# Optimization experiments

Measured on AMD Instinct MI355X. Metric: run time of the kernel, lower is better.

The kernel has to match this reference:

```python
import jax, jax.numpy as jnp
import numpy as np

CHANNELS = 512
NUM_HEADS = 8
NUM_GROUPS = 32
EPS = 1e-5


def setup_inputs() -> dict:
    key = jax.random.key(0)
    ks = jax.random.split(key, 6)
    c = CHANNELS
    x = jax.random.normal(ks[0], (8, c, 32, 32), dtype=jnp.float32)
    norm_w = jnp.ones((c,), jnp.float32)
    norm_b = jnp.zeros((c,), jnp.float32)
    # 1x1 conv1d weights stored as [out, in]
    qkv_w = jax.random.normal(ks[1], (3 * c, c), jnp.float32) * (1.0 / np.sqrt(c))
    qkv_b = jax.random.normal(ks[2], (3 * c,), jnp.float32) * 0.02
    # proj_out is zero-initialized in the original; use small random values so the
    # residual branch is exercised numerically (init values are not part of the math).
    proj_w = jax.random.normal(ks[3], (c, c), jnp.float32) * 0.02
    proj_b = jax.random.normal(ks[4], (c,), jnp.float32) * 0.02
    return {"x": x, "norm_w": norm_w, "norm_b": norm_b,
            "qkv_w": qkv_w, "qkv_b": qkv_b, "proj_w": proj_w, "proj_b": proj_b}


def _group_norm(x, w, b):
    # x: [B, C, L]; normalize per (batch, group) over (C/G, L) in float32
    B, C, L = x.shape
    xg = x.astype(jnp.float32).reshape(B, NUM_GROUPS, (C // NUM_GROUPS) * L)
    mean = xg.mean(axis=-1, keepdims=True)
    var = xg.var(axis=-1, keepdims=True)
    xn = ((xg - mean) * jax.lax.rsqrt(var + EPS)).reshape(B, C, L)
    return (xn * w[None, :, None] + b[None, :, None]).astype(x.dtype)


def _attention_legacy(qkv, n_heads):
    # qkv: [B, 3*C, L]  (QKVAttentionLegacy: split heads after reshape)
    B, width, L = qkv.shape
    ch = width // (3 * n_heads)
    q, k, v = jnp.split(qkv.reshape(B * n_heads, 3 * ch, L), 3, axis=1)
    scale = 1.0 / np.sqrt(np.sqrt(ch))
    w = jnp.einsum('bct,bcs->bts', q * scale, k * scale)  # [B*H, L, L]
    w = jax.nn.softmax(w.astype(jnp.float32), axis=-1).astype(qkv.dtype)
    a = jnp.einsum('bts,bcs->bct', w, v)  # [B*H, ch, L]
    return a.reshape(B, n_heads * ch, L)


def reference(x, norm_w, norm_b, qkv_w, qkv_b, proj_w, proj_b):
    b, c = x.shape[0], x.shape[1]
    spatial = x.shape[2:]
    x_ = x.reshape(b, c, -1)  # [B, C, L]
    xn = _group_norm(x_, norm_w, norm_b)
    qkv = jnp.einsum('oc,bcl->bol', qkv_w, xn) + qkv_b[None, :, None]
    h = _attention_legacy(qkv, NUM_HEADS)
    h = jnp.einsum('oc,bcl->bol', proj_w, h) + proj_b[None, :, None]
    return (x_ + h).reshape(b, c, *spatial)
```

## Files before the change

### kernel.cpp

```cpp
#include <hip/hip_runtime.h>
#include <hip/hip_bf16.h>
#include <stdint.h>


#define NB 8
#define NC 512
#define NL 1024
#define NHD 8
#define ND 64

typedef __attribute__((ext_vector_type(4))) float f32x4;
typedef __attribute__((ext_vector_type(8))) short bf16x8;
typedef __attribute__((ext_vector_type(4))) short bf16x4;
typedef __attribute__((ext_vector_type(4))) unsigned short u16x4;
typedef __attribute__((ext_vector_type(8))) unsigned short u16x8;

#define MFMA16(a, b, c) __builtin_amdgcn_mfma_f32_16x16x32_bf16((a), (b), (c), 0, 0, 0)

static __device__ __forceinline__ f32x4 mfma_k16(bf16x4 a, bf16x4 b, f32x4 c) {
#if __has_builtin(__builtin_amdgcn_mfma_f32_16x16x16bf16_1k)
  return __builtin_amdgcn_mfma_f32_16x16x16bf16_1k(a, b, c, 0, 0, 0);
#else
  asm("v_mfma_f32_16x16x16_bf16 %0, %1, %2, %0" : "+v"(c) : "v"(a), "v"(b));
  return c;
#endif
}

#if __has_builtin(__builtin_amdgcn_exp2f)
#define EXP2F __builtin_amdgcn_exp2f
#else
#define EXP2F exp2f
#endif

static __device__ __forceinline__ unsigned short f2bf(float f) {
  union { float f; uint32_t u; } v; v.f = f;
  uint32_t r = v.u + 0x7fffu + ((v.u >> 16) & 1u);
  return (unsigned short)(r >> 16);
}

static __device__ __forceinline__ short f2bf_h(float f) {
  __hip_bfloat16 h = __float2bfloat16(f);
  return *reinterpret_cast<short*>(&h);
}

static __device__ __forceinline__ void gl_lds16(const unsigned short* g, unsigned short* l) {
  __builtin_amdgcn_global_load_lds(
      (const __attribute__((address_space(1))) void*)g,
      (__attribute__((address_space(3))) void*)l, 16, 0, 0);
}

__global__ __launch_bounds__(256) void k_pre(const float* __restrict__ x,
                                             const float* __restrict__ nw,
                                             const float* __restrict__ nb,
                                             const float* __restrict__ qkvw,
                                             const float* __restrict__ pw,
                                             unsigned short* __restrict__ xnt,
                                             unsigned short* __restrict__ qwb,
                                             unsigned short* __restrict__ pwb) {
  if (blockIdx.x >= 256) {
    int i = (blockIdx.x - 256) * 256 + threadIdx.x;
    const int NQ4 = (3 * NC * NC) / 4;
    if (i < NQ4) {
      f32x4 v = ((const f32x4*)qkvw)[i];
      u16x4 o; o.x = f2bf(v.x); o.y = f2bf(v.y); o.z = f2bf(v.z); o.w = f2bf(v.w);
      ((u16x4*)qwb)[i] = o;
    } else {
      int j = i - NQ4;
      f32x4 v = ((const f32x4*)pw)[j];
      u16x4 o; o.x = f2bf(v.x); o.y = f2bf(v.y); o.z = f2bf(v.z); o.w = f2bf(v.w);
      ((u16x4*)pwb)[j] = o;
    }
    return;
  }
  const int b = blockIdx.x >> 5, g = blockIdx.x & 31;
  const float* base = x + ((size_t)b * NC + g * 16) * NL;
  const int t = threadIdx.x;
  f32x4 vals[16];
  float s = 0.f, ss = 0.f;
#pragma unroll
  for (int r = 0; r < 16; ++r) {
    f32x4 v = ((const f32x4*)base)[t + 256 * r];
    vals[r] = v;
    s += v.x + v.y + v.z + v.w;
    ss += v.x * v.x + v.y * v.y + v.z * v.z + v.w * v.w;
  }
#pragma unroll
  for (int m = 1; m < 64; m <<= 1) { s += __shfl_xor(s, m, 64); ss += __shfl_xor(ss, m, 64); }
  __shared__ float red[8];
  const int w = t >> 6;
  if ((t & 63) == 0) { red[w] = s; red[4 + w] = ss; }
  __syncthreads();
  s  = red[0] + red[1] + red[2] + red[3];
  ss = red[4] + red[5] + red[6] + red[7];
  const float mean = s * (1.f / 16384.f);
  const float var  = ss * (1.f / 16384.f) - mean * mean;
  const float inv  = rsqrtf(var + 1e-5f);
  u16x8 ov[4][2];
#pragma unroll
  for (int r = 0; r < 16; ++r) {
    float wcv = nw[g * 16 + r] * inv;
    float bcv = nb[g * 16 + r] - mean * wcv;
    f32x4 v = vals[r];
    ov[0][r >> 3][r & 7] = f2bf(v.x * wcv + bcv);
    ov[1][r >> 3][r & 7] = f2bf(v.y * wcv + bcv);
    ov[2][r >> 3][r & 7] = f2bf(v.z * wcv + bcv);
    ov[3][r >> 3][r & 7] = f2bf(v.w * wcv + bcv);
  }
#pragma unroll
  for (int j = 0; j < 4; ++j) {
    size_t off = ((size_t)b * NL + 4 * t + j) * NC + g * 16;
    *(u16x8*)(xnt + off)     = ov[j][0];
    *(u16x8*)(xnt + off + 8) = ov[j][1];
  }
}

__global__ __launch_bounds__(256) void k_qkv(const unsigned short* __restrict__ xnt,
                                             const unsigned short* __restrict__ qwb,
                                             const float* __restrict__ qkvb,
                                             unsigned short* __restrict__ qt,
                                             unsigned short* __restrict__ kt,
                                             unsigned short* __restrict__ vt) {
  __shared__ __align__(16) unsigned short As[128 * 64];
  __shared__ __align__(16) unsigned short Bs[128 * 64];
  const int m0 = blockIdx.x * 128;
  const int n0 = blockIdx.y * 128;
  const int b = blockIdx.z;
  const int tid = threadIdx.x, lane = tid & 63, w = tid >> 6;
  const int wr = w >> 1, wc = w & 1;

  int soff[4];
#pragma unroll
  for (int r = 0; r < 4; ++r) {
    int c = (r * 4 + w) * 64 + lane;
    int row = c >> 3, lc = (c & 7) ^ (row & 7);
    soff[r] = row * NC + lc * 8;
  }
  const unsigned short* Ap = xnt + (size_t)b * NL * NC + (size_t)m0 * NC;
  const unsigned short* Bp = qwb + (size_t)n0 * NC;

  f32x4 acc[4][4];
#pragma unroll
  for (int mi = 0; mi < 4; ++mi)
#pragma unroll
    for (int ni = 0; ni < 4; ++ni) acc[mi][ni] = (f32x4){0.f, 0.f, 0.f, 0.f};

  for (int k0 = 0; k0 < NC; k0 += 64) {
#pragma unroll
    for (int r = 0; r < 4; ++r) gl_lds16(Ap + soff[r], &As[(r * 4 + w) * 512]);
#pragma unroll
    for (int r = 0; r < 4; ++r) gl_lds16(Bp + soff[r], &Bs[(r * 4 + w) * 512]);
    Ap += 64; Bp += 64;
    __syncthreads();
#pragma unroll
    for (int ks = 0; ks < 2; ++ks) {
      bf16x8 af[4], bfr[4];
#pragma unroll
      for (int mi = 0; mi < 4; ++mi) {
        int row = wr * 64 + mi * 16 + (lane & 15);
        int ph = ((lane >> 4) + ks * 4) ^ (row & 7);
        af[mi] = *(const bf16x8*)&As[row * 64 + ph * 8];
      }
#pragma unroll
      for (int ni = 0; ni < 4; ++ni) {
        int row = wc * 64 + ni * 16 + (lane & 15);
        int ph = ((lane >> 4) + ks * 4) ^ (row & 7);
        bfr[ni] = *(const bf16x8*)&Bs[row * 64 + ph * 8];
      }
#pragma unroll
      for (int mi = 0; mi < 4; ++mi)
#pragma unroll
        for (int ni = 0; ni < 4; ++ni)
          acc[mi][ni] = MFMA16(af[mi], bfr[ni], acc[mi][ni]);
    }
    __syncthreads();
  }
#pragma unroll
  for (int ni = 0; ni < 4; ++ni) {
    int o = n0 + wc * 64 + ni * 16 + (lane & 15);
    int head = o / 192, rem = o - head * 192;
    int type = rem >> 6, ch = rem & 63;
    float bias = qkvb[o];
#pragma unroll
    for (int mi = 0; mi < 4; ++mi) {
      int l0 = m0 + wr * 64 + mi * 16 + ((lane >> 4) << 2);
      if (type == 2) {
        u16x4 pk;
#pragma unroll
        for (int i = 0; i < 4; ++i) pk[i] = f2bf(acc[mi][ni][i] + bias);
        *(u16x4*)&vt[(((size_t)(b * NHD + head) * 256 + (l0 >> 2)) * ND + ch) * 4] = pk;
      } else {
        const float sc = (type == 0)
            ? (0.35355339059327373f * 1.4426950408889634f)
            : 0.35355339059327373f;
        unsigned short* dst =
            (type == 0 ? qt : kt) + ((size_t)(b * NHD + head) * NL + l0) * ND + ch;
#pragma unroll
        for (int i = 0; i < 4; ++i)
          dst[i * ND] = f2bf((acc[mi][ni][i] + bias) * sc);
      }
    }
  }
}

__global__ __launch_bounds__(256) void k_attn(const unsigned short* __restrict__ qt,
                                              const unsigned short* __restrict__ kt,
                                              const unsigned short* __restrict__ vt,
                                              unsigned short* __restrict__ abuf) {
  __shared__ __align__(16) unsigned short Ks[2][128 * 64];
  __shared__ __align__(16) unsigned short Vs[2][128 * 64];
  const int bid = blockIdx.x;
  const int bh = (bid & 7) * 8 + (bid >> 6);
  const int tb = (bid >> 3) & 7;
  const int tid = threadIdx.x, lane = tid & 63, w = tid >> 6;
  const int lo = lane & 15, g = lane >> 4;
  const int t0 = tb * 128 + w * 32;
  const unsigned short* qb = qt + (size_t)bh * NL * ND;

  int koff[4], voff[4];
#pragma unroll
  for (int r = 0; r < 4; ++r) {
    int c = (r * 4 + w) * 64 + lane;
    int row = c >> 3, lc = (c & 7) ^ (row & 7);
    koff[r] = row * ND + lc * 8;
    voff[r] = c * 8;
  }
  const int e0 = lo * 64 + ((g ^ (lo & 7)) * 8);
  const int e1 = lo * 64 + (((4 + g) ^ (lo & 7)) * 8);
  const int vbase = g * 256 + lo * 4;

  const unsigned short* kst = kt + (size_t)bh * NL * ND;
  const unsigned short* vst = vt + (size_t)bh * NL * ND;

  bf16x8 qf[2][2];
#pragma unroll
  for (int h = 0; h < 2; ++h)
#pragma unroll
    for (int ks = 0; ks < 2; ++ks)
      qf[h][ks] = *(const bf16x8*)&qb[(size_t)(t0 + h * 16 + lo) * ND + ks * 32 + g * 8];

  bf16x4 vones;
#pragma unroll
  for (int j = 0; j < 4; ++j) vones[j] = (short)0x3F80;

  f32x4 pv[2][4];
#pragma unroll
  for (int h = 0; h < 2; ++h)
#pragma unroll
    for (int ci = 0; ci < 4; ++ci) pv[h][ci] = (f32x4){0.f, 0.f, 0.f, 0.f};
  f32x4 lacc[2];
  lacc[0] = (f32x4){0.f, 0.f, 0.f, 0.f};
  lacc[1] = (f32x4){0.f, 0.f, 0.f, 0.f};

#pragma unroll
  for (int r = 0; r < 4; ++r) {
    gl_lds16(kst + koff[r], &Ks[0][(r * 4 + w) * 512]);
    gl_lds16(vst + voff[r], &Vs[0][(r * 4 + w) * 512]);
  }
  kst += 8192; vst += 8192;

#define ATTN_HALF(BUF, HH)                                                    \
  {                                                                           \
    f32x4 sacc[2][4];                                                         \
    _Pragma("unroll")                                                         \
    for (int h = 0; h < 2; ++h)                                               \
      _Pragma("unroll")                                                       \
      for (int sblk = 0; sblk < 4; ++sblk)                                    \
        sacc[h][sblk] = (f32x4){0.f, 0.f, 0.f, 0.f};                          \
    __builtin_amdgcn_s_setprio(1);                                            \
    _Pragma("unroll")                                                         \
    for (int sblk = 0; sblk < 4; ++sblk) {                                    \
      bf16x8 kf = *(const bf16x8*)&Ks[BUF][(HH) * 4096 + sblk * 1024 + e0];   \
      sacc[0][sblk] = MFMA16(kf, qf[0][0], sacc[0][sblk]);                    \
      sacc[1][sblk] = MFMA16(kf, qf[1][0], sacc[1][sblk]);                    \
    }                                                                         \
    _Pragma("unroll")                                                         \
    for (int sblk = 0; sblk < 4; ++sblk) {                                    \
      bf16x8 kf = *(const bf16x8*)&Ks[BUF][(HH) * 4096 + sblk * 1024 + e1];   \
      sacc[0][sblk] = MFMA16(kf, qf[0][1], sacc[0][sblk]);                    \
      sacc[1][sblk] = MFMA16(kf, qf[1][1], sacc[1][sblk]);                    \
    }                                                                         \
    __builtin_amdgcn_s_setprio(0);                                            \
    _Pragma("unroll")                                                         \
    for (int sblk = 0; sblk < 4; ++sblk) {                                    \
      float a0 = EXP2F(sacc[0][sblk][0]);                                     \
      float a1 = EXP2F(sacc[0][sblk][1]);                                     \
      float a2 = EXP2F(sacc[0][sblk][2]);                                     \
      float a3 = EXP2F(sacc[0][sblk][3]);                                     \
      bf16x4 pf0;                                                             \
      pf0[0] = f2bf_h(a0); pf0[1] = f2bf_h(a1);                               \
      pf0[2] = f2bf_h(a2); pf0[3] = f2bf_h(a3);                               \
      float b0 = EXP2F(sacc[1][sblk][0]);                                     \
      float b1 = EXP2F(sacc[1][sblk][1]);                                     \
      float b2 = EXP2F(sacc[1][sblk][2]);                                     \
      float b3 = EXP2F(sacc[1][sblk][3]);                                     \
      bf16x4 pf1;                                                             \
      pf1[0] = f2bf_h(b0); pf1[1] = f2bf_h(b1);                               \
      pf1[2] = f2bf_h(b2); pf1[3] = f2bf_h(b3);                               \
      __builtin_amdgcn_s_setprio(1);                                          \
      lacc[0] = mfma_k16(pf0, vones, lacc[0]);                                \
      lacc[1] = mfma_k16(pf1, vones, lacc[1]);                                \
      _Pragma("unroll")                                                       \
      for (int ci = 0; ci < 4; ++ci) {                                        \
        bf16x4 vf = *(const bf16x4*)                                          \
            &Vs[BUF][(HH) * 4096 + sblk * 1024 + ci * 64 + vbase];            \
        pv[0][ci] = mfma_k16(pf0, vf, pv[0][ci]);                             \
        pv[1][ci] = mfma_k16(pf1, vf, pv[1][ci]);                             \
      }                                                                       \
      __builtin_amdgcn_s_setprio(0);                                          \
    }                                                                         \
  }

#define ATTN_TILE(BUF, LAST)                                                  \
  {                                                                           \
    __syncthreads();                                                          \
    if (!(LAST)) {                                                            \
      _Pragma("unroll")                                                       \
      for (int r = 0; r < 4; ++r)                                             \
        gl_lds16(kst + koff[r], &Ks[(BUF) ^ 1][(r * 4 + w) * 512]);           \
    }                                                                         \
    ATTN_HALF(BUF, 0);                                                        \
    if (!(LAST)) {                                                            \
      _Pragma("unroll")                                                       \
      for (int r = 0; r < 4; ++r)                                             \
        gl_lds16(vst + voff[r], &Vs[(BUF) ^ 1][(r * 4 + w) * 512]);           \
      kst += 8192; vst += 8192;                                               \
    }                                                                         \
    ATTN_HALF(BUF, 1);                                                        \
  }

  for (int it = 0; it < 8; it += 2) {
    ATTN_TILE(0, false);
    ATTN_TILE(1, it == 6);
  }
#undef ATTN_TILE
#undef ATTN_HALF

#pragma unroll
  for (int h = 0; h < 2; ++h) {
    float li[4];
#pragma unroll
    for (int i = 0; i < 4; ++i) li[i] = 1.0f / lacc[h][i];
#pragma unroll
    for (int ci = 0; ci < 4; ++ci)
#pragma unroll
      for (int i = 0; i < 4; ++i) {
        int tl = t0 + h * 16 + g * 4 + i;
        abuf[((size_t)bh * NL + tl) * ND + ci * 16 + lo] = f2bf_h(pv[h][ci][i] * li[i]);
      }
  }
}

__global__ __launch_bounds__(256) void k_proj(const unsigned short* __restrict__ abuf,
                                              const unsigned short* __restrict__ pwb,
                                              const float* __restrict__ pb,
                                              const float* __restrict__ x,
                                              float* __restrict__ out) {
  __shared__ __align__(16) unsigned short As[128 * 64];
  __shared__ __align__(16) unsigned short Bs[128 * 64];
  const int m0 = blockIdx.x * 128;
  const int n0 = blockIdx.y * 128;
  const int b = blockIdx.z;
  const int tid = threadIdx.x, lane = tid & 63, w = tid >> 6;
  const int wr = w >> 1, wc = w & 1;

  int aoff[4], boff[4];
#pragma unroll
  for (int r = 0; r < 4; ++r) {
    int c = (r * 4 + w) * 64 + lane;
    int row = c >> 3, lc = (c & 7) ^ (row & 7);
    aoff[r] = row * NC + lc * 8;
    boff[r] = row * ND + lc * 8;
  }
  const unsigned short* Ap = pwb + (size_t)m0 * NC;
  const unsigned short* Bp = abuf + ((size_t)(b * NHD) * NL + n0) * ND;

  f32x4 acc[4][4];
#pragma unroll
  for (int mi = 0; mi < 4; ++mi)
#pragma unroll
    for (int ni = 0; ni < 4; ++ni) acc[mi][ni] = (f32x4){0.f, 0.f, 0.f, 0.f};

  for (int k0 = 0; k0 < NC; k0 += 64) {
#pragma unroll
    for (int r = 0; r < 4; ++r) gl_lds16(Ap + aoff[r], &As[(r * 4 + w) * 512]);
#pragma unroll
    for (int r = 0; r < 4; ++r) gl_lds16(Bp + boff[r], &Bs[(r * 4 + w) * 512]);
    Ap += 64; Bp += (size_t)NL * ND;
    __syncthreads();
#pragma unroll
    for (int ks = 0; ks < 2; ++ks) {
      bf16x8 af[4], bfr[4];
#pragma unroll
      for (int mi = 0; mi < 4; ++mi) {
        int row = wr * 64 + mi * 16 + (lane & 15);
        int ph = ((lane >> 4) + ks * 4) ^ (row & 7);
        af[mi] = *(const bf16x8*)&As[row * 64 + ph * 8];
      }
#pragma unroll
      for (int ni = 0; ni < 4; ++ni) {
        int row = wc * 64 + ni * 16 + (lane & 15);
        int ph = ((lane >> 4) + ks * 4) ^ (row & 7);
        bfr[ni] = *(const bf16x8*)&Bs[row * 64 + ph * 8];
      }
#pragma unroll
      for (int mi = 0; mi < 4; ++mi)
#pragma unroll
        for (int ni = 0; ni < 4; ++ni)
          acc[mi][ni] = MFMA16(af[mi], bfr[ni], acc[mi][ni]);
    }
    __syncthreads();
  }
#pragma unroll
  for (int mi = 0; mi < 4; ++mi)
#pragma unroll
    for (int i = 0; i < 4; ++i) {
      int o = m0 + wr * 64 + mi * 16 + ((lane >> 4) << 2) + i;
      float pbv = pb[o];
#pragma unroll
      for (int ni = 0; ni < 4; ++ni) {
        int l = n0 + wc * 64 + ni * 16 + (lane & 15);
        size_t idx = ((size_t)b * NC + o) * NL + l;
        out[idx] = x[idx] + acc[mi][ni][i] + pbv;
      }
    }
}

extern "C" void kernel_launch(void* const* d_in, const int* in_sizes, int n_in,
                              void* d_out, int out_size, void* d_ws, size_t ws_size,
                              hipStream_t stream) {
  const float* x    = (const float*)d_in[0];
  const float* nw   = (const float*)d_in[1];
  const float* nb   = (const float*)d_in[2];
  const float* qkvw = (const float*)d_in[3];
  const float* qkvb = (const float*)d_in[4];
  const float* pw   = (const float*)d_in[5];
  const float* pb   = (const float*)d_in[6];
  float* out = (float*)d_out;

  char* ws = (char*)d_ws;
  unsigned short* xnt  = (unsigned short*)(ws);
  unsigned short* abuf = (unsigned short*)(ws);
  unsigned short* qwb  = (unsigned short*)(ws + 8388608);
  unsigned short* pwb  = (unsigned short*)(ws + 9961472);
  unsigned short* qt   = (unsigned short*)(ws + 10485760);
  unsigned short* kt   = (unsigned short*)(ws + 18874368);
  unsigned short* vt   = (unsigned short*)(ws + 27262976);

  k_pre<<<1280, 256, 0, stream>>>(x, nw, nb, qkvw, pw, xnt, qwb, pwb);
  k_qkv<<<dim3(8, 12, 8), 256, 0, stream>>>(xnt, qwb, qkvb, qt, kt, vt);
  k_attn<<<512, 256, 0, stream>>>(qt, kt, vt, abuf);
  k_proj<<<dim3(4, 8, 8), 256, 0, stream>>>(abuf, pwb, pb, x, out);
}
```

Before: 79.53 us.

## Double-buffer LDS tiles in QKV and projection GEMMs to overlap loads

Both the QKV and output-projection GEMM kernels now keep two LDS buffers per operand. Global-to-LDS loads for the next K-slice are issued between the MFMA sub-steps on the current buffer, and only one barrier is used per K step. The goal is to hide global load latency behind MFMA work. The cost is twice the LDS per block (64 KB), which may reduce occupancy.

```diff
diff --git a/kernel.cpp b/kernel.cpp
--- a/kernel.cpp
+++ b/kernel.cpp
@@ -120,13 +120,14 @@
                                              unsigned short* __restrict__ qt,
                                              unsigned short* __restrict__ kt,
                                              unsigned short* __restrict__ vt) {
-  __shared__ __align__(16) unsigned short As[128 * 64];
-  __shared__ __align__(16) unsigned short Bs[128 * 64];
+  __shared__ __align__(16) unsigned short As[2][128 * 64];
+  __shared__ __align__(16) unsigned short Bs[2][128 * 64];
   const int m0 = blockIdx.x * 128;
   const int n0 = blockIdx.y * 128;
   const int b = blockIdx.z;
   const int tid = threadIdx.x, lane = tid & 63, w = tid >> 6;
   const int wr = w >> 1, wc = w & 1;
+  const int lo = lane & 15, g = lane >> 4;
 
   int soff[4];
 #pragma unroll
@@ -144,45 +145,69 @@
 #pragma unroll
     for (int ni = 0; ni < 4; ++ni) acc[mi][ni] = (f32x4){0.f, 0.f, 0.f, 0.f};
 
-  for (int k0 = 0; k0 < NC; k0 += 64) {
-#pragma unroll
-    for (int r = 0; r < 4; ++r) gl_lds16(Ap + soff[r], &As[(r * 4 + w) * 512]);
-#pragma unroll
-    for (int r = 0; r < 4; ++r) gl_lds16(Bp + soff[r], &Bs[(r * 4 + w) * 512]);
-    Ap += 64; Bp += 64;
-    __syncthreads();
-#pragma unroll
-    for (int ks = 0; ks < 2; ++ks) {
-      bf16x8 af[4], bfr[4];
-#pragma unroll
-      for (int mi = 0; mi < 4; ++mi) {
-        int row = wr * 64 + mi * 16 + (lane & 15);
-        int ph = ((lane >> 4) + ks * 4) ^ (row & 7);
-        af[mi] = *(const bf16x8*)&As[row * 64 + ph * 8];
-      }
-#pragma unroll
-      for (int ni = 0; ni < 4; ++ni) {
-        int row = wc * 64 + ni * 16 + (lane & 15);
-        int ph = ((lane >> 4) + ks * 4) ^ (row & 7);
-        bfr[ni] = *(const bf16x8*)&Bs[row * 64 + ph * 8];
-      }
-#pragma unroll
-      for (int mi = 0; mi < 4; ++mi)
-#pragma unroll
-        for (int ni = 0; ni < 4; ++ni)
-          acc[mi][ni] = MFMA16(af[mi], bfr[ni], acc[mi][ni]);
-    }
-    __syncthreads();
-  }
+#pragma unroll
+  for (int r = 0; r < 4; ++r) {
+    gl_lds16(Ap + soff[r], &As[0][(r * 4 + w) * 512]);
+    gl_lds16(Bp + soff[r], &Bs[0][(r * 4 + w) * 512]);
+  }
+  Ap += 64; Bp += 64;
+
+#define QKV_KS(BUF, KS)                                                       \
+  {                                                                           \
+    bf16x8 af[4], bfr[4];                                                     \
+    _Pragma("unroll")                                                         \
+    for (int mi = 0; mi < 4; ++mi) {                                          \
+      int row = wr * 64 + mi * 16 + lo;                                       \
+      int ph = (g + (KS) * 4) ^ (row & 7);                                    \
+      af[mi] = *(const bf16x8*)&As[BUF][row * 64 + ph * 8];                   \
+    }                                                                         \
+    _Pragma("unroll")                                                         \
+    for (int ni = 0; ni < 4; ++ni) {                                          \
+      int row = wc * 64 + ni * 16 + lo;                                       \
+      int ph = (g + (KS) * 4) ^ (row & 7);                                    \
+      bfr[ni] = *(const bf16x8*)&Bs[BUF][row * 64 + ph * 8];                  \
+    }                                                                         \
+    _Pragma("unroll")                                                         \
+    for (int mi = 0; mi < 4; ++mi)                                            \
+      _Pragma("unroll")                                                       \
+      for (int ni = 0; ni < 4; ++ni)                                          \
+        acc[mi][ni] = MFMA16(af[mi], bfr[ni], acc[mi][ni]);                   \
+  }
+
+#define QKV_STEP(BUF, LAST)                                                   \
+  {                                                                           \
+    __syncthreads();                                                          \
+    if (!(LAST)) {                                                            \
+      _Pragma("unroll")                                                       \
+      for (int r = 0; r < 4; ++r)                                             \
+        gl_lds16(Ap + soff[r], &As[(BUF) ^ 1][(r * 4 + w) * 512]);            \
+    }                                                                         \
+    QKV_KS(BUF, 0);                                                           \
+    if (!(LAST)) {                                                            \
+      _Pragma("unroll")                                                       \
+      for (int r = 0; r < 4; ++r)                                             \
+        gl_lds16(Bp + soff[r], &Bs[(BUF) ^ 1][(r * 4 + w) * 512]);            \
+      Ap += 64; Bp += 64;                                                     \
+    }                                                                         \
+    QKV_KS(BUF, 1);                                                           \
+  }
+
+  for (int it = 0; it < 8; it += 2) {
+    QKV_STEP(0, false);
+    QKV_STEP(1, it == 6);
+  }
+#undef QKV_STEP
+#undef QKV_KS
+
 #pragma unroll
   for (int ni = 0; ni < 4; ++ni) {
-    int o = n0 + wc * 64 + ni * 16 + (lane & 15);
+    int o = n0 + wc * 64 + ni * 16 + lo;
     int head = o / 192, rem = o - head * 192;
     int type = rem >> 6, ch = rem & 63;
     float bias = qkvb[o];
 #pragma unroll
     for (int mi = 0; mi < 4; ++mi) {
-      int l0 = m0 + wr * 64 + mi * 16 + ((lane >> 4) << 2);
+      int l0 = m0 + wr * 64 + mi * 16 + (g << 2);
       if (type == 2) {
         u16x4 pk;
 #pragma unroll
@@ -355,13 +380,14 @@
                                               const float* __restrict__ pb,
                                               const float* __restrict__ x,
                                               float* __restrict__ out) {
-  __shared__ __align__(16) unsigned short As[128 * 64];
-  __shared__ __align__(16) unsigned short Bs[128 * 64];
+  __shared__ __align__(16) unsigned short As[2][128 * 64];
+  __shared__ __align__(16) unsigned short Bs[2][128 * 64];
   const int m0 = blockIdx.x * 128;
   const int n0 = blockIdx.y * 128;
   const int b = blockIdx.z;
   const int tid = threadIdx.x, lane = tid & 63, w = tid >> 6;
   const int wr = w >> 1, wc = w & 1;
+  const int lo = lane & 15, g = lane >> 4;
 
   int aoff[4], boff[4];
 #pragma unroll
@@ -380,45 +406,69 @@
 #pragma unroll
     for (int ni = 0; ni < 4; ++ni) acc[mi][ni] = (f32x4){0.f, 0.f, 0.f, 0.f};
 
-  for (int k0 = 0; k0 < NC; k0 += 64) {
-#pragma unroll
-    for (int r = 0; r < 4; ++r) gl_lds16(Ap + aoff[r], &As[(r * 4 + w) * 512]);
-#pragma unroll
-    for (int r = 0; r < 4; ++r) gl_lds16(Bp + boff[r], &Bs[(r * 4 + w) * 512]);
-    Ap += 64; Bp += (size_t)NL * ND;
-    __syncthreads();
-#pragma unroll
-    for (int ks = 0; ks < 2; ++ks) {
-      bf16x8 af[4], bfr[4];
-#pragma unroll
-      for (int mi = 0; mi < 4; ++mi) {
-        int row = wr * 64 + mi * 16 + (lane & 15);
-        int ph = ((lane >> 4) + ks * 4) ^ (row & 7);
-        af[mi] = *(const bf16x8*)&As[row * 64 + ph * 8];
-      }
+#pragma unroll
+  for (int r = 0; r < 4; ++r) {
+    gl_lds16(Ap + aoff[r], &As[0][(r * 4 + w) * 512]);
+    gl_lds16(Bp + boff[r], &Bs[0][(r * 4 + w) * 512]);
+  }
+  Ap += 64; Bp += (size_t)NL * ND;
+
+#define PROJ_KS(BUF, KS)                                                      \
+  {                                                                           \
+    bf16x8 af[4], bfr[4];                                                     \
+    _Pragma("unroll")                                                         \
+    for (int mi = 0; mi < 4; ++mi) {                                          \
+      int row = wr * 64 + mi * 16 + lo;                                       \
+      int ph = (g + (KS) * 4) ^ (row & 7);                                    \
+      af[mi] = *(const bf16x8*)&As[BUF][row * 64 + ph * 8];                   \
+    }                                                                         \
+    _Pragma("unroll")                                                         \
+    for (int ni = 0; ni < 4; ++ni) {                                          \
+      int row = wc * 64 + ni * 16 + lo;                                       \
+      int ph = (g + (KS) * 4) ^ (row & 7);                                    \
+      bfr[ni] = *(const bf16x8*)&Bs[BUF][row * 64 + ph * 8];                  \
+    }                                                                         \
+    _Pragma("unroll")                                                         \
+    for (int mi = 0; mi < 4; ++mi)                                            \
+      _Pragma("unroll")                                                       \
+      for (int ni = 0; ni < 4; ++ni)                                          \
+        acc[mi][ni] = MFMA16(af[mi], bfr[ni], acc[mi][ni]);                   \
+  }
+
+#define PROJ_STEP(BUF, LAST)                                                  \
+  {                                                                           \
+    __syncthreads();                                                          \
+    if (!(LAST)) {                                                            \
+      _Pragma("unroll")                                                       \
+      for (int r = 0; r < 4; ++r)                                             \
+        gl_lds16(Ap + aoff[r], &As[(BUF) ^ 1][(r * 4 + w) * 512]);            \
+    }                                                                         \
+    PROJ_KS(BUF, 0);                                                          \
+    if (!(LAST)) {                                                            \
+      _Pragma("unroll")                                                       \
+      for (int r = 0; r < 4; ++r)                                             \
+        gl_lds16(Bp + boff[r], &Bs[(BUF) ^ 1][(r * 4 + w) * 512]);            \
+      Ap += 64; Bp += (size_t)NL * ND;                                        \
+    }                                                                         \
+    PROJ_KS(BUF, 1);                                                          \
+  }
+
+  for (int it = 0; it < 8; it += 2) {
+    PROJ_STEP(0, false);
+    PROJ_STEP(1, it == 6);
+  }
+#undef PROJ_STEP
+#undef PROJ_KS
+
+#pragma unroll
+  for (int mi = 0; mi < 4; ++mi)
+#pragma unroll
+    for (int i = 0; i < 4; ++i) {
+      int o = m0 + wr * 64 + mi * 16 + g * 4 + i;
+      float pbv = pb[o];
 #pragma unroll
       for (int ni = 0; ni < 4; ++ni) {
-        int row = wc * 64 + ni * 16 + (lane & 15);
-        int ph = ((lane >> 4) + ks * 4) ^ (row & 7);
-        bfr[ni] = *(const bf16x8*)&Bs[row * 64 + ph * 8];
-      }
-#pragma unroll
-      for (int mi = 0; mi < 4; ++mi)
-#pragma unroll
-        for (int ni = 0; ni < 4; ++ni)
-          acc[mi][ni] = MFMA16(af[mi], bfr[ni], acc[mi][ni]);
-    }
-    __syncthreads();
-  }
-#pragma unroll
-  for (int mi = 0; mi < 4; ++mi)
-#pragma unroll
-    for (int i = 0; i < 4; ++i) {
-      int o = m0 + wr * 64 + mi * 16 + ((lane >> 4) << 2) + i;
-      float pbv = pb[o];
-#pragma unroll
-      for (int ni = 0; ni < 4; ++ni) {
-        int l = n0 + wc * 64 + ni * 16 + (lane & 15);
+        int l = n0 + wc * 64 + ni * 16 + lo;
         size_t idx = ((size_t)b * NC + o) * NL + l;
         out[idx] = x[idx] + acc[mi][ni][i] + pbv;
       }
```

New measurement: 77.78 us (median of 2 runs). -2.2%, faster.
